# Performance work log

Hardware: AMD Instinct MI355X
Metric: run time of the kernel (lower is better)

The kernel has to match this reference:

```python
import jax, jax.numpy as jnp
import numpy as np

B, T, D, H = 4, 2048, 1024, 16
Hd = D // H


def setup_inputs() -> dict:
    key = jax.random.key(0)
    ks = jax.random.split(key, 6)
    s = 1.0 / np.sqrt(D)
    return {
        "x": jax.random.normal(ks[0], (B, T, D), dtype=jnp.float32),
        "mask": jnp.zeros((B, T), dtype=bool),
        "Wq": jax.random.normal(ks[1], (D, D), dtype=jnp.float32) * s,
        "bq": jnp.zeros((D,), dtype=jnp.float32),
        "Wk": jax.random.normal(ks[2], (D, D), dtype=jnp.float32) * s,
        "bk": jnp.zeros((D,), dtype=jnp.float32),
        "Wv": jax.random.normal(ks[3], (D, D), dtype=jnp.float32) * s,
        "bv": jnp.zeros((D,), dtype=jnp.float32),
        "Wo": jax.random.normal(ks[4], (D, D), dtype=jnp.float32) * s,
        "bo": jnp.zeros((D,), dtype=jnp.float32),
    }


def reference(x, mask, Wq, bq, Wk, bk, Wv, bv, Wo, bo):
    b, t, d = x.shape
    # projections -> [B, T, H, Hd]
    Q = (x @ Wq + bq).reshape(b, t, H, Hd)
    K = (x @ Wk + bk).reshape(b, t, H, Hd)
    V = (x @ Wv + bv).reshape(b, t, H, Hd)
    scale = jnp.asarray(Hd, x.dtype) ** -0.5
    # full score matrix [B, H, Tq, Tk] (matches the naive torch impl)
    attn = jnp.einsum("bqhd,bkhd->bhqk", Q, K) * scale
    attn = jnp.where(mask[:, None, None, :], jnp.asarray(-1e9, attn.dtype), attn)
    attn = jax.nn.softmax(attn, axis=-1)
    out = jnp.einsum("bhqk,bkhd->bqhd", attn, V).reshape(b, t, d)
    return out @ Wo + bo
```

## Files before the change

### kernel.cpp

```cpp
#include <hip/hip_runtime.h>

using bf16 = __bf16;
typedef bf16 bf16x4 __attribute__((ext_vector_type(4)));
typedef bf16 bf16x8 __attribute__((ext_vector_type(8)));
typedef float f32x4 __attribute__((ext_vector_type(4)));
typedef float f32x8 __attribute__((ext_vector_type(8)));

#define MFMA16(a, b, c) __builtin_amdgcn_mfma_f32_16x16x32_bf16(a, b, c, 0, 0, 0)

constexpr int Bb = 4, Tt = 2048, Dd = 1024, Hh = 16, Hd = 64;
constexpr int Mrows = Bb * Tt;
constexpr float CEXP = 0.18033688011112042f;

__global__ void cast_f32_bf16_kernel(const float* __restrict__ in, bf16* __restrict__ out) {
  size_t i = ((size_t)blockIdx.x * 256 + threadIdx.x) * 8;
  f32x8 v = *(const f32x8*)(in + i);
  *(bf16x8*)(out + i) = __builtin_convertvector(v, bf16x8);
}

__global__ void transpose_cast_w_kernel(const float* __restrict__ W, bf16* __restrict__ Wt,
                                        float scale) {
  __shared__ alignas(16) float tile[64][68];
  const int tid = threadIdx.x;
  const int n0 = blockIdx.x * 64, k0 = blockIdx.y * 64;
#pragma unroll
  for (int it = 0; it < 4; ++it) {
    int chunk = tid + it * 256;
    int kr = chunk >> 4, c4 = chunk & 15;
    f32x4 v = *(const f32x4*)(W + (size_t)(k0 + kr) * Dd + n0 + c4 * 4);
    *(f32x4*)&tile[kr][c4 * 4] = v * scale;
  }
  __syncthreads();
#pragma unroll
  for (int it = 0; it < 2; ++it) {
    int chunk = tid + it * 256;
    int n = chunk & 63, k8 = chunk >> 6;
    bf16x8 o;
#pragma unroll
    for (int j = 0; j < 8; ++j) o[j] = (bf16)tile[k8 * 8 + j][n];
    *(bf16x8*)(Wt + (size_t)(n0 + n) * Dd + k0 + k8 * 8) = o;
  }
}

__global__ void pack_bias_kernel(const float* __restrict__ bq, const float* __restrict__ bk,
                                 const float* __restrict__ bv, float* __restrict__ outb) {
  int i = blockIdx.x * 256 + threadIdx.x;
  float v = (i < 1024) ? bq[i] * CEXP : (i < 2048 ? bk[i - 1024] : bv[i - 2048]);
  outb[i] = v;
}

template <typename OutT>
__global__ __launch_bounds__(256)
void gemm_bf16_kernel(const bf16* __restrict__ A, const bf16* __restrict__ Bt,
                      const float* __restrict__ bias, OutT* __restrict__ C,
                      int M, int N, int K) {
  __shared__ alignas(16) bf16 As[128][72];
  __shared__ alignas(16) bf16 Bs[128][72];
  const int tid = threadIdx.x;
  const int lane = tid & 63, wave = tid >> 6;
  const int col = lane & 15, quad = lane >> 4;
  const int wr = (wave >> 1) * 64, wc = (wave & 1) * 64;
  const size_t m0 = (size_t)blockIdx.x * 128, n0 = (size_t)blockIdx.y * 128;

  f32x4 acc[4][4];
#pragma unroll
  for (int i = 0; i < 4; ++i)
#pragma unroll
    for (int j = 0; j < 4; ++j)
#pragma unroll
      for (int r = 0; r < 4; ++r) acc[i][j][r] = 0.f;

  for (int k0 = 0; k0 < K; k0 += 64) {
#pragma unroll
    for (int it = 0; it < 4; ++it) {
      int chunk = tid + it * 256;
      int rr = chunk >> 3, c8 = chunk & 7;
      *(bf16x8*)&As[rr][c8 * 8] = *(const bf16x8*)(A + (m0 + rr) * (size_t)K + k0 + c8 * 8);
      *(bf16x8*)&Bs[rr][c8 * 8] = *(const bf16x8*)(Bt + (n0 + rr) * (size_t)K + k0 + c8 * 8);
    }
    __syncthreads();
#pragma unroll
    for (int kk = 0; kk < 2; ++kk) {
      bf16x8 af[4], bfr[4];
#pragma unroll
      for (int i = 0; i < 4; ++i) af[i] = *(const bf16x8*)&As[wr + i * 16 + col][kk * 32 + quad * 8];
#pragma unroll
      for (int j = 0; j < 4; ++j) bfr[j] = *(const bf16x8*)&Bs[wc + j * 16 + col][kk * 32 + quad * 8];
#pragma unroll
      for (int i = 0; i < 4; ++i)
#pragma unroll
        for (int j = 0; j < 4; ++j) acc[i][j] = MFMA16(af[i], bfr[j], acc[i][j]);
    }
    __syncthreads();
  }
#pragma unroll
  for (int i = 0; i < 4; ++i)
#pragma unroll
    for (int j = 0; j < 4; ++j) {
      size_t row = m0 + wr + i * 16 + quad * 4;
      size_t c = n0 + wc + j * 16 + col;
      float bv = bias[c];
#pragma unroll
      for (int r = 0; r < 4; ++r) C[(row + r) * (size_t)N + c] = (OutT)(acc[i][j][r] + bv);
    }
}

__global__ void transpose_v_kernel(const bf16* __restrict__ qkv, bf16* __restrict__ vt) {
  __shared__ alignas(16) bf16 tile[64][72];
  const int tid = threadIdx.x;
  const int t0 = blockIdx.x * 64;
  const int h = blockIdx.y, b = blockIdx.z;
  const bf16* src = qkv + (size_t)(b * Tt + t0) * 3072 + 2048 + h * Hd;
#pragma unroll
  for (int it = 0; it < 2; ++it) {
    int chunk = tid + it * 256;
    int tr = chunk >> 3, d8 = chunk & 7;
    bf16x8 v = *(const bf16x8*)(src + (size_t)tr * 3072 + d8 * 8);
#pragma unroll
    for (int j = 0; j < 8; ++j) tile[d8 * 8 + j][tr] = v[j];
  }
  __syncthreads();
  bf16* dst = vt + ((size_t)(b * Hh + h) * Hd) * Tt + t0;
#pragma unroll
  for (int it = 0; it < 2; ++it) {
    int chunk = tid + it * 256;
    int d = chunk >> 3, t8 = chunk & 7;
    bf16x8 o = *(const bf16x8*)&tile[d][t8 * 8];
    *(bf16x8*)(dst + (size_t)d * Tt + t8 * 8) = o;
  }
}

__global__ __launch_bounds__(256, 2)
void flash_attn_kernel(const bf16* __restrict__ qkv, const bf16* __restrict__ vt,
                       const unsigned char* __restrict__ mask, bf16* __restrict__ ao) {
  __shared__ alignas(16) bf16 Ks[2][64 * 64];
  __shared__ alignas(16) bf16 Vs[2][64 * 64];
  __shared__ alignas(16) bf16 pbuf[4][16 * 64];

  const int tid = threadIdx.x;
  const int wave = tid >> 6, lane = tid & 63;
  const int col = lane & 15, quad = lane >> 4;
  const int id = blockIdx.x;
  const int hb = id & 63, qi2 = id >> 6;
  const int h = hb & 15, b = hb >> 4;
  const int qbase0 = qi2 * 256 + wave * 64;

  const bf16* Qp = qkv + (size_t)(b * Tt) * 3072 + h * Hd;
  const bf16* Kp = Qp + 1024;
  const bf16* Vp = vt + ((size_t)(b * Hh + h) * Hd) * Tt;
  const unsigned char* mp = mask + b * Tt;

  unsigned long long anym;
  {
    const unsigned long long* mq = (const unsigned long long*)mp;
    unsigned long long acc = 0;
#pragma unroll
    for (int j = 0; j < 4; ++j) acc |= mq[lane * 4 + j];
    anym = __ballot(acc != 0ull);
  }

  bf16x8 qf[4][2];
#pragma unroll
  for (int t = 0; t < 4; ++t)
#pragma unroll
    for (int kk = 0; kk < 2; ++kk)
      qf[t][kk] = *(const bf16x8*)(Qp + (size_t)(qbase0 + t * 16 + col) * 3072 + kk * 32 + quad * 8);

  const bf16* Ksrc = Kp + (size_t)lane * 3072 + wave * 16;
  const bf16* Vsrc = Vp + (size_t)lane * Tt + wave * 16;
  const int ss1 = ((2 * wave) ^ (lane & 7)) * 8;
  const int ss2 = ((2 * wave + 1) ^ (lane & 7)) * 8;
  const int srowoff = lane * 64;

  {
    bf16x8 k0 = *(const bf16x8*)Ksrc, k1 = *(const bf16x8*)(Ksrc + 8);
    bf16x8 v0 = *(const bf16x8*)Vsrc, v1 = *(const bf16x8*)(Vsrc + 8);
    *(bf16x8*)&Ks[0][srowoff + ss1] = k0;  *(bf16x8*)&Ks[0][srowoff + ss2] = k1;
    *(bf16x8*)&Vs[0][srowoff + ss1] = v0;  *(bf16x8*)&Vs[0][srowoff + ss2] = v1;
  }
  __syncthreads();

  f32x4 oacc[4][4];
  float lsum[4];
#pragma unroll
  for (int t = 0; t < 4; ++t) {
    lsum[t] = 0.f;
#pragma unroll
    for (int n = 0; n < 4; ++n)
#pragma unroll
      for (int r = 0; r < 4; ++r) oacc[t][n][r] = 0.f;
  }

  const int fslot0 = ((0 * 4 + quad) ^ (col & 7)) * 8;
  const int fslot1 = ((1 * 4 + quad) ^ (col & 7)) * 8;

  for (int i = 0; i < 32; ++i) {
    const int cur = i & 1, nxt = cur ^ 1;
    const int kb = i * 64;

    bf16x8 nk0, nk1, nv0, nv1;
    if (i < 31) {
      const bf16* ks = Ksrc + (size_t)(kb + 64) * 3072;
      const bf16* vs = Vsrc + (kb + 64);
      nk0 = *(const bf16x8*)ks;  nk1 = *(const bf16x8*)(ks + 8);
      nv0 = *(const bf16x8*)vs;  nv1 = *(const bf16x8*)(vs + 8);
    }

    bf16x8 kf[4][2], vf[4][2];
#pragma unroll
    for (int kt = 0; kt < 4; ++kt) {
      kf[kt][0] = *(const bf16x8*)&Ks[cur][(kt * 16 + col) * 64 + fslot0];
      kf[kt][1] = *(const bf16x8*)&Ks[cur][(kt * 16 + col) * 64 + fslot1];
    }
#pragma unroll
    for (int n = 0; n < 4; ++n) {
      vf[n][0] = *(const bf16x8*)&Vs[cur][(n * 16 + col) * 64 + fslot0];
      vf[n][1] = *(const bf16x8*)&Vs[cur][(n * 16 + col) * 64 + fslot1];
    }

#pragma unroll
    for (int t = 0; t < 4; ++t) {
      f32x4 s[4];
#pragma unroll
      for (int kt = 0; kt < 4; ++kt)
#pragma unroll
        for (int r = 0; r < 4; ++r) s[kt][r] = 0.f;
#pragma unroll
      for (int kk = 0; kk < 2; ++kk)
#pragma unroll
        for (int kt = 0; kt < 4; ++kt) s[kt] = MFMA16(kf[kt][kk], qf[t][kk], s[kt]);

      if ((anym >> (2 * i)) & 3ull) {
#pragma unroll
        for (int kt = 0; kt < 4; ++kt)
#pragma unroll
          for (int r = 0; r < 4; ++r)
            if (mp[kb + kt * 16 + quad * 4 + r] != 0) s[kt][r] = -1e9f;
      }

      float rs = 0.f;
#pragma unroll
      for (int kt = 0; kt < 4; ++kt) {
        bf16x4 pk;
#pragma unroll
        for (int r = 0; r < 4; ++r) {
          float p = __builtin_amdgcn_exp2f(s[kt][r]);
          rs += p;
          pk[r] = (bf16)p;
        }
        int slot = ((2 * kt + (quad >> 1)) ^ (col & 7)) * 8 + (quad & 1) * 4;
        *(bf16x4*)&pbuf[wave][col * 64 + slot] = pk;
      }
      __builtin_amdgcn_s_waitcnt(0xc07f);
      bf16x8 pf0 = *(const bf16x8*)&pbuf[wave][col * 64 + fslot0];
      bf16x8 pf1 = *(const bf16x8*)&pbuf[wave][col * 64 + fslot1];
#pragma unroll
      for (int n = 0; n < 4; ++n) {
        oacc[t][n] = MFMA16(vf[n][0], pf0, oacc[t][n]);
        oacc[t][n] = MFMA16(vf[n][1], pf1, oacc[t][n]);
      }
      rs += __shfl_xor(rs, 16, 64);
      rs += __shfl_xor(rs, 32, 64);
      lsum[t] += rs;
    }

    if (i < 31) {
      *(bf16x8*)&Ks[nxt][srowoff + ss1] = nk0;  *(bf16x8*)&Ks[nxt][srowoff + ss2] = nk1;
      *(bf16x8*)&Vs[nxt][srowoff + ss1] = nv0;  *(bf16x8*)&Vs[nxt][srowoff + ss2] = nv1;
    }
    __syncthreads();
  }

#pragma unroll
  for (int t = 0; t < 4; ++t) {
    float rl = 1.0f / lsum[t];
    size_t q = (size_t)b * Tt + qbase0 + t * 16 + col;
#pragma unroll
    for (int n = 0; n < 4; ++n) {
      bf16x4 ov;
#pragma unroll
      for (int r = 0; r < 4; ++r) ov[r] = (bf16)(oacc[t][n][r] * rl);
      *(bf16x4*)(ao + q * Dd + h * Hd + n * 16 + quad * 4) = ov;
    }
  }
}

extern "C" void kernel_launch(void* const* d_in, const int* in_sizes, int n_in,
                              void* d_out, int out_size, void* d_ws, size_t ws_size,
                              hipStream_t stream) {
  const float* x = (const float*)d_in[0];
  const unsigned char* mask = (const unsigned char*)d_in[1];
  const float* Wq = (const float*)d_in[2];
  const float* bq = (const float*)d_in[3];
  const float* Wk = (const float*)d_in[4];
  const float* bk = (const float*)d_in[5];
  const float* Wv = (const float*)d_in[6];
  const float* bv = (const float*)d_in[7];
  const float* Wo = (const float*)d_in[8];
  const float* bo = (const float*)d_in[9];
  float* out = (float*)d_out;

  char* ws = (char*)d_ws;
  size_t off = 0;
  auto alloc = [&](size_t bytes) {
    char* p = ws + off;
    off += (bytes + 255) & ~(size_t)255;
    return p;
  };
  bf16* xb  = (bf16*)alloc((size_t)Mrows * Dd * 2);
  bf16* Wt  = (bf16*)alloc((size_t)3 * Dd * Dd * 2);
  bf16* Wot = (bf16*)alloc((size_t)Dd * Dd * 2);
  bf16* QKV = (bf16*)alloc((size_t)Mrows * 3 * Dd * 2);
  bf16* Vt  = (bf16*)alloc((size_t)Bb * Hh * Hd * Tt * 2);
  float* bqkv = (float*)alloc((size_t)3 * Dd * 4);

  cast_f32_bf16_kernel<<<Mrows * Dd / (256 * 8), 256, 0, stream>>>(x, xb);
  transpose_cast_w_kernel<<<dim3(16, 16), 256, 0, stream>>>(Wq, Wt, CEXP);
  transpose_cast_w_kernel<<<dim3(16, 16), 256, 0, stream>>>(Wk, Wt + (size_t)Dd * Dd, 1.0f);
  transpose_cast_w_kernel<<<dim3(16, 16), 256, 0, stream>>>(Wv, Wt + (size_t)2 * Dd * Dd, 1.0f);
  transpose_cast_w_kernel<<<dim3(16, 16), 256, 0, stream>>>(Wo, Wot, 1.0f);
  pack_bias_kernel<<<12, 256, 0, stream>>>(bq, bk, bv, bqkv);

  gemm_bf16_kernel<bf16><<<dim3(Mrows / 128, 3 * Dd / 128), 256, 0, stream>>>(
      xb, Wt, bqkv, QKV, Mrows, 3 * Dd, Dd);
  transpose_v_kernel<<<dim3(Tt / 64, Hh, Bb), 256, 0, stream>>>(QKV, Vt);

  bf16* AO = xb;
  flash_attn_kernel<<<dim3(512), 256, 0, stream>>>(QKV, Vt, mask, AO);
  gemm_bf16_kernel<float><<<dim3(Mrows / 128, Dd / 128), 256, 0, stream>>>(
      AO, Wot, bo, out, Mrows, Dd, Dd);
}
```

Baseline: 297.5 us.

## Use direct global-to-LDS loads in GEMM, batch softmax P stores, merge weight casts

The GEMM tile loads now go straight from global memory into LDS through global_load_lds. This skips the round trip through registers, but it drops the padded layout, so LDS bank conflicts may appear on the MFMA fragment reads. The attention kernel gives each wave four P buffers, computes and stores all four query sub-tiles before one wait, then runs the PV MFMAs. That removes the per-sub-tile wait but uses more LDS, which may reduce occupancy. The four weight transpose-cast launches are merged into one 3D launch.

New measurement: 300.9 us. No clear change (+1.2%).

```diff
diff --git a/kernel.cpp b/kernel.cpp
--- a/kernel.cpp
+++ b/kernel.cpp
@@ -12,17 +12,27 @@
 constexpr int Mrows = Bb * Tt;
 constexpr float CEXP = 0.18033688011112042f;
 
+__device__ __forceinline__ void gload_lds16(const bf16* g, bf16* lds_base) {
+  __builtin_amdgcn_global_load_lds((const __attribute__((address_space(1))) void*)g,
+                                   (__attribute__((address_space(3))) void*)lds_base,
+                                   16, 0, 0);
+}
+
 __global__ void cast_f32_bf16_kernel(const float* __restrict__ in, bf16* __restrict__ out) {
   size_t i = ((size_t)blockIdx.x * 256 + threadIdx.x) * 8;
   f32x8 v = *(const f32x8*)(in + i);
   *(bf16x8*)(out + i) = __builtin_convertvector(v, bf16x8);
 }
 
-__global__ void transpose_cast_w_kernel(const float* __restrict__ W, bf16* __restrict__ Wt,
-                                        float scale) {
+__global__ void transpose_cast_w4_kernel(const float* __restrict__ Wq, const float* __restrict__ Wk,
+                                         const float* __restrict__ Wv, const float* __restrict__ Wo,
+                                         bf16* __restrict__ Wt, bf16* __restrict__ Wot) {
   __shared__ alignas(16) float tile[64][68];
   const int tid = threadIdx.x;
-  const int n0 = blockIdx.x * 64, k0 = blockIdx.y * 64;
+  const int n0 = blockIdx.x * 64, k0 = blockIdx.y * 64, z = blockIdx.z;
+  const float* W = (z == 0) ? Wq : (z == 1) ? Wk : (z == 2) ? Wv : Wo;
+  bf16* dst = (z == 3) ? Wot : (Wt + (size_t)z * Dd * Dd);
+  const float scale = (z == 0) ? CEXP : 1.0f;
 #pragma unroll
   for (int it = 0; it < 4; ++it) {
     int chunk = tid + it * 256;
@@ -38,7 +48,7 @@
     bf16x8 o;
 #pragma unroll
     for (int j = 0; j < 8; ++j) o[j] = (bf16)tile[k8 * 8 + j][n];
-    *(bf16x8*)(Wt + (size_t)(n0 + n) * Dd + k0 + k8 * 8) = o;
+    *(bf16x8*)(dst + (size_t)(n0 + n) * Dd + k0 + k8 * 8) = o;
   }
 }
 
@@ -54,13 +64,14 @@
 void gemm_bf16_kernel(const bf16* __restrict__ A, const bf16* __restrict__ Bt,
                       const float* __restrict__ bias, OutT* __restrict__ C,
                       int M, int N, int K) {
-  __shared__ alignas(16) bf16 As[128][72];
-  __shared__ alignas(16) bf16 Bs[128][72];
+  __shared__ alignas(16) bf16 As[128 * 64];
+  __shared__ alignas(16) bf16 Bs[128 * 64];
   const int tid = threadIdx.x;
   const int lane = tid & 63, wave = tid >> 6;
   const int col = lane & 15, quad = lane >> 4;
   const int wr = (wave >> 1) * 64, wc = (wave & 1) * 64;
   const size_t m0 = (size_t)blockIdx.x * 128, n0 = (size_t)blockIdx.y * 128;
+  const int srow = lane >> 3, schunk = (lane & 7) * 8;
 
   f32x4 acc[4][4];
 #pragma unroll
@@ -73,19 +84,18 @@
   for (int k0 = 0; k0 < K; k0 += 64) {
 #pragma unroll
     for (int it = 0; it < 4; ++it) {
-      int chunk = tid + it * 256;
-      int rr = chunk >> 3, c8 = chunk & 7;
-      *(bf16x8*)&As[rr][c8 * 8] = *(const bf16x8*)(A + (m0 + rr) * (size_t)K + k0 + c8 * 8);
-      *(bf16x8*)&Bs[rr][c8 * 8] = *(const bf16x8*)(Bt + (n0 + rr) * (size_t)K + k0 + c8 * 8);
+      int rbase = it * 32 + wave * 8;
+      gload_lds16(A + (m0 + rbase + srow) * (size_t)K + k0 + schunk, &As[rbase * 64]);
+      gload_lds16(Bt + (n0 + rbase + srow) * (size_t)K + k0 + schunk, &Bs[rbase * 64]);
     }
     __syncthreads();
 #pragma unroll
     for (int kk = 0; kk < 2; ++kk) {
       bf16x8 af[4], bfr[4];
 #pragma unroll
-      for (int i = 0; i < 4; ++i) af[i] = *(const bf16x8*)&As[wr + i * 16 + col][kk * 32 + quad * 8];
-#pragma unroll
-      for (int j = 0; j < 4; ++j) bfr[j] = *(const bf16x8*)&Bs[wc + j * 16 + col][kk * 32 + quad * 8];
+      for (int i = 0; i < 4; ++i) af[i] = *(const bf16x8*)&As[(wr + i * 16 + col) * 64 + kk * 32 + quad * 8];
+#pragma unroll
+      for (int j = 0; j < 4; ++j) bfr[j] = *(const bf16x8*)&Bs[(wc + j * 16 + col) * 64 + kk * 32 + quad * 8];
 #pragma unroll
       for (int i = 0; i < 4; ++i)
 #pragma unroll
@@ -135,7 +145,7 @@
                        const unsigned char* __restrict__ mask, bf16* __restrict__ ao) {
   __shared__ alignas(16) bf16 Ks[2][64 * 64];
   __shared__ alignas(16) bf16 Vs[2][64 * 64];
-  __shared__ alignas(16) bf16 pbuf[4][16 * 64];
+  __shared__ alignas(16) bf16 pbuf[4][4][16 * 64];
 
   const int tid = threadIdx.x;
   const int wave = tid >> 6, lane = tid & 63;
@@ -218,6 +228,7 @@
       vf[n][1] = *(const bf16x8*)&Vs[cur][(n * 16 + col) * 64 + fslot1];
     }
 
+    float rsv[4];
 #pragma unroll
     for (int t = 0; t < 4; ++t) {
       f32x4 s[4];
@@ -241,27 +252,32 @@
       float rs = 0.f;
 #pragma unroll
       for (int kt = 0; kt < 4; ++kt) {
-        bf16x4 pk;
+        f32x4 pv;
 #pragma unroll
         for (int r = 0; r < 4; ++r) {
-          float p = __builtin_amdgcn_exp2f(s[kt][r]);
-          rs += p;
-          pk[r] = (bf16)p;
+          pv[r] = __builtin_amdgcn_exp2f(s[kt][r]);
+          rs += pv[r];
         }
+        bf16x4 pk = __builtin_convertvector(pv, bf16x4);
         int slot = ((2 * kt + (quad >> 1)) ^ (col & 7)) * 8 + (quad & 1) * 4;
-        *(bf16x4*)&pbuf[wave][col * 64 + slot] = pk;
+        *(bf16x4*)&pbuf[wave][t][col * 64 + slot] = pk;
       }
-      __builtin_amdgcn_s_waitcnt(0xc07f);
-      bf16x8 pf0 = *(const bf16x8*)&pbuf[wave][col * 64 + fslot0];
-      bf16x8 pf1 = *(const bf16x8*)&pbuf[wave][col * 64 + fslot1];
+      rs += __shfl_xor(rs, 16, 64);
+      rs += __shfl_xor(rs, 32, 64);
+      rsv[t] = rs;
+    }
+
+    __builtin_amdgcn_s_waitcnt(0xc07f);
+#pragma unroll
+    for (int t = 0; t < 4; ++t) {
+      bf16x8 pf0 = *(const bf16x8*)&pbuf[wave][t][col * 64 + fslot0];
+      bf16x8 pf1 = *(const bf16x8*)&pbuf[wave][t][col * 64 + fslot1];
 #pragma unroll
       for (int n = 0; n < 4; ++n) {
         oacc[t][n] = MFMA16(vf[n][0], pf0, oacc[t][n]);
         oacc[t][n] = MFMA16(vf[n][1], pf1, oacc[t][n]);
       }
-      rs += __shfl_xor(rs, 16, 64);
-      rs += __shfl_xor(rs, 32, 64);
-      lsum[t] += rs;
+      lsum[t] += rsv[t];
     }
 
     if (i < 31) {
@@ -315,10 +331,7 @@
   float* bqkv = (float*)alloc((size_t)3 * Dd * 4);
 
   cast_f32_bf16_kernel<<<Mrows * Dd / (256 * 8), 256, 0, stream>>>(x, xb);
-  transpose_cast_w_kernel<<<dim3(16, 16), 256, 0, stream>>>(Wq, Wt, CEXP);
-  transpose_cast_w_kernel<<<dim3(16, 16), 256, 0, stream>>>(Wk, Wt + (size_t)Dd * Dd, 1.0f);
-  transpose_cast_w_kernel<<<dim3(16, 16), 256, 0, stream>>>(Wv, Wt + (size_t)2 * Dd * Dd, 1.0f);
-  transpose_cast_w_kernel<<<dim3(16, 16), 256, 0, stream>>>(Wo, Wot, 1.0f);
+  transpose_cast_w4_kernel<<<dim3(16, 16, 4), 256, 0, stream>>>(Wq, Wk, Wv, Wo, Wt, Wot);
   pack_bias_kernel<<<12, 256, 0, stream>>>(bq, bk, bv, bqkv);
 
   gemm_bf16_kernel<bf16><<<dim3(Mrows / 128, 3 * Dd / 128), 256, 0, stream>>>(
```
